# Performance work log

Measured on AMD Instinct MI355X. Metric: run time of the kernel, lower is better.

The kernel has to match this reference:

```python
import jax, jax.numpy as jnp
import numpy as np

TOP_K = 4


def setup_inputs() -> dict:
    key = jax.random.key(0)
    k1, k2, k3 = jax.random.split(key, 3)
    T, H, E = 16384, 2880, 128
    hidden_states = jax.random.normal(k1, (T, H), dtype=jnp.float32)
    weight = jax.random.normal(k2, (E, H), dtype=jnp.float32) * 0.02
    bias = jax.random.normal(k3, (E,), dtype=jnp.float32) * 0.02
    return {"hidden_states": hidden_states, "weight": weight, "bias": bias}


def reference(hidden_states, weight, bias):
    # [T, H] @ [H, E] + [E] -> router logits [T, E]
    hidden_states = hidden_states.reshape(-1, weight.shape[1])
    router_logits = jnp.einsum('th,eh->te', hidden_states, weight) + bias
    # top-k over experts, then softmax over the k selected logits
    router_top_value, router_indices = jax.lax.top_k(router_logits, TOP_K)
    router_scores = jax.nn.softmax(router_top_value, axis=-1)
    return router_scores, router_indices
```

## Files before the change

### kernel.cpp

```cpp
#include <hip/hip_runtime.h>
#include <hip/hip_bf16.h>
#include <math.h>

#define T_TOKENS 16384
#define H_DIM    2880
#define KHALF    1440
#define E_EXP    128
#define TOPK     4
#define MT       32
#define KC       32
#define EPS_GAP  5e-4f

typedef __bf16 bf16x8 __attribute__((ext_vector_type(8)));
typedef float  f32x4  __attribute__((ext_vector_type(4)));

__device__ __forceinline__ void split2(float a, float b,
                                       unsigned int& hi, unsigned int& lo) {
    float2 p; p.x = a; p.y = b;
    __hip_bfloat162 h = __float22bfloat162_rn(p);
    unsigned int hu; __builtin_memcpy(&hu, &h, 4);
    float2 r;
    r.x = a - __uint_as_float((hu & 0xffffu) << 16);
    r.y = b - __uint_as_float(hu & 0xffff0000u);
    __hip_bfloat162 l = __float22bfloat162_rn(r);
    unsigned int lu; __builtin_memcpy(&lu, &l, 4);
    hi = hu; lo = lu;
}

__global__ __launch_bounds__(512, 4) void router_main(
    const float* __restrict__ A, const float* __restrict__ W,
    const float* __restrict__ bias, float* __restrict__ out,
    int* __restrict__ flag_count, int* __restrict__ flag_list)
{
    __shared__ __align__(16) uint2 sAhi[2][2][128];
    __shared__ __align__(16) uint2 sAlo[2][2][128];
    __shared__ __align__(16) uint4 sWhi[2][8][64];
    __shared__ __align__(16) uint4 sWlo[2][8][64];
    __shared__ float sL[MT][129];

    const int tid    = threadIdx.x;
    const int t_base = blockIdx.x * MT;

    const int wave  = tid >> 6;
    const int L     = tid & 63;
    const int whalf = wave >> 2;
    const int wm    = wave & 1;
    const int wn    = (wave >> 1) & 1;

    const int shalf = tid >> 8;
    const int tid_h = tid & 255;
    const int at = tid_h >> 3;
    const int ac = tid_h & 7;
    const int a_idx = (at >> 4) * 128 + ((((ac >> 1) << 4) | (at & 15)) << 1) + (ac & 1);
    const float* Ag = A + (size_t)(t_base + at) * H_DIM + shalf * KHALF + ac * 4;
    const int we  = tid_h >> 1;
    const int wq0 = (tid_h & 1) * 2;
    const float* Wg = W + (size_t)we * H_DIM + shalf * KHALF + wq0 * 8;
    const int w_nt = we >> 4;
    const int w_n  = we & 15;

    uint2* sAhiF = &sAhi[shalf][0][0];
    uint2* sAloF = &sAlo[shalf][0][0];

    f32x4 acc[4];
#pragma unroll
    for (int i = 0; i < 4; ++i) { f32x4 z = {0.f, 0.f, 0.f, 0.f}; acc[i] = z; }

    for (int k0 = 0; k0 < KHALF; k0 += KC) {
        const float4 av  = *(const float4*)(Ag + k0);
        const float4 wv0 = *(const float4*)(Wg + k0);
        const float4 wv1 = *(const float4*)(Wg + k0 + 4);
        const float4 wv2 = *(const float4*)(Wg + k0 + 8);
        const float4 wv3 = *(const float4*)(Wg + k0 + 12);

        uint2 ahp, alp;
        split2(av.x, av.y, ahp.x, alp.x);
        split2(av.z, av.w, ahp.y, alp.y);

        uint4 whp0, wlp0, whp1, wlp1;
        split2(wv0.x, wv0.y, whp0.x, wlp0.x);
        split2(wv0.z, wv0.w, whp0.y, wlp0.y);
        split2(wv1.x, wv1.y, whp0.z, wlp0.z);
        split2(wv1.z, wv1.w, whp0.w, wlp0.w);
        split2(wv2.x, wv2.y, whp1.x, wlp1.x);
        split2(wv2.z, wv2.w, whp1.y, wlp1.y);
        split2(wv3.x, wv3.y, whp1.z, wlp1.z);
        split2(wv3.z, wv3.w, whp1.w, wlp1.w);

        __syncthreads();

        sAhiF[a_idx] = ahp;
        sAloF[a_idx] = alp;
        sWhi[shalf][w_nt][((wq0 + 0) << 4) | w_n] = whp0;
        sWhi[shalf][w_nt][((wq0 + 1) << 4) | w_n] = whp1;
        sWlo[shalf][w_nt][((wq0 + 0) << 4) | w_n] = wlp0;
        sWlo[shalf][w_nt][((wq0 + 1) << 4) | w_n] = wlp1;

        __syncthreads();

        const bf16x8 ahi = *(const bf16x8*)&sAhi[whalf][wm][L * 2];
        const bf16x8 alo = *(const bf16x8*)&sAlo[whalf][wm][L * 2];
#pragma unroll
        for (int i = 0; i < 4; ++i) {
            const int nt = wn * 4 + i;
            const bf16x8 whi = *(const bf16x8*)&sWhi[whalf][nt][L];
            const bf16x8 wlo = *(const bf16x8*)&sWlo[whalf][nt][L];
            acc[i] = __builtin_amdgcn_mfma_f32_16x16x32_bf16(ahi, whi, acc[i], 0, 0, 0);
            acc[i] = __builtin_amdgcn_mfma_f32_16x16x32_bf16(ahi, wlo, acc[i], 0, 0, 0);
            acc[i] = __builtin_amdgcn_mfma_f32_16x16x32_bf16(alo, whi, acc[i], 0, 0, 0);
        }
    }

    __syncthreads();
    if (whalf == 0) {
#pragma unroll
        for (int i = 0; i < 4; ++i) {
            const int e = wn * 64 + i * 16 + (L & 15);
            const float b = bias[e];
#pragma unroll
            for (int r = 0; r < 4; ++r)
                sL[wm * 16 + (L >> 4) * 4 + r][e] = acc[i][r] + b;
        }
    }
    __syncthreads();
    if (whalf == 1) {
#pragma unroll
        for (int i = 0; i < 4; ++i) {
            const int e = wn * 64 + i * 16 + (L & 15);
#pragma unroll
            for (int r = 0; r < 4; ++r)
                sL[wm * 16 + (L >> 4) * 4 + r][e] += acc[i][r];
        }
    }
    __syncthreads();

    if (tid < MT) {
        float v0 = -1e30f, v1 = -1e30f, v2 = -1e30f, v3 = -1e30f, v4 = -1e30f;
        int   i0 = 0, i1 = 0, i2 = 0, i3 = 0, i4 = 0;
        for (int e = 0; e < E_EXP; ++e) {
            const float x = sL[tid][e];
            if (x > v4) {
                if (x > v0)      { v4=v3;i4=i3; v3=v2;i3=i2; v2=v1;i2=i1; v1=v0;i1=i0; v0=x;i0=e; }
                else if (x > v1) { v4=v3;i4=i3; v3=v2;i3=i2; v2=v1;i2=i1; v1=x;i1=e; }
                else if (x > v2) { v4=v3;i4=i3; v3=v2;i3=i2; v2=x;i2=e; }
                else if (x > v3) { v4=v3;i4=i3; v3=x;i3=e; }
                else             { v4=x;i4=e; }
            }
        }
        const float g0 = v0 - v1, g1 = v1 - v2, g2 = v2 - v3, g3 = v3 - v4;
        float mg = g0 < g1 ? g0 : g1;
        mg = mg < g2 ? mg : g2;
        mg = mg < g3 ? mg : g3;

        const float e0x = expf(v0 - v0);
        const float e1x = expf(v1 - v0);
        const float e2x = expf(v2 - v0);
        const float e3x = expf(v3 - v0);
        const float s   = e0x + e1x + e2x + e3x;

        const int gt = t_base + tid;
        float* out_scores = out;
        float* out_idx    = out + (size_t)T_TOKENS * TOPK;
        out_scores[gt * 4 + 0] = e0x / s;
        out_scores[gt * 4 + 1] = e1x / s;
        out_scores[gt * 4 + 2] = e2x / s;
        out_scores[gt * 4 + 3] = e3x / s;
        out_idx[gt * 4 + 0] = (float)i0;
        out_idx[gt * 4 + 1] = (float)i1;
        out_idx[gt * 4 + 2] = (float)i2;
        out_idx[gt * 4 + 3] = (float)i3;

        if (mg < EPS_GAP) {
            const int p = atomicAdd(flag_count, 1);
            if (p < T_TOKENS) flag_list[p] = gt;
        }
    }
}

__global__ __launch_bounds__(256) void router_recheck(
    const float* __restrict__ A, const float* __restrict__ W,
    const float* __restrict__ bias, float* __restrict__ out,
    const int* __restrict__ flag_count, const int* __restrict__ flag_list)
{
    __shared__ double sPart[256];
    __shared__ double sLog[E_EXP];

    int count = *flag_count;
    if (count > T_TOKENS) count = T_TOKENS;

    const int tid = threadIdx.x;
    const int e   = tid & (E_EXP - 1);
    const int h   = tid >> 7;

    for (int i = blockIdx.x; i < count; i += gridDim.x) {
        const int t = flag_list[i];
        const float* arow = A + (size_t)t * H_DIM;
        const float* wrow = W + (size_t)e * H_DIM;
        const int k0 = h * (H_DIM / 2);

        double s0 = 0.0, s1 = 0.0, s2 = 0.0, s3 = 0.0;
        for (int k = k0; k < k0 + H_DIM / 2; k += 8) {
            const float4 a0 = *(const float4*)(arow + k);
            const float4 a1 = *(const float4*)(arow + k + 4);
            const float4 w0 = *(const float4*)(wrow + k);
            const float4 w1 = *(const float4*)(wrow + k + 4);
            s0 += (double)a0.x * (double)w0.x;
            s1 += (double)a0.y * (double)w0.y;
            s2 += (double)a0.z * (double)w0.z;
            s3 += (double)a0.w * (double)w0.w;
            s0 += (double)a1.x * (double)w1.x;
            s1 += (double)a1.y * (double)w1.y;
            s2 += (double)a1.z * (double)w1.z;
            s3 += (double)a1.w * (double)w1.w;
        }
        sPart[tid] = (s0 + s1) + (s2 + s3);
        __syncthreads();
        if (h == 0) sLog[e] = sPart[e] + sPart[e + 128] + (double)bias[e];
        __syncthreads();

        if (tid == 0) {
            double v0 = -1e300, v1 = -1e300, v2 = -1e300, v3 = -1e300;
            int    i0 = 0, i1 = 0, i2 = 0, i3 = 0;
            for (int q = 0; q < E_EXP; ++q) {
                const double x = sLog[q];
                if (x > v3) {
                    if (x > v0)      { v3=v2;i3=i2; v2=v1;i2=i1; v1=v0;i1=i0; v0=x;i0=q; }
                    else if (x > v1) { v3=v2;i3=i2; v2=v1;i2=i1; v1=x;i1=q; }
                    else if (x > v2) { v3=v2;i3=i2; v2=x;i2=q; }
                    else             { v3=x;i3=q; }
                }
            }
            const double e0x = exp(v0 - v0);
            const double e1x = exp(v1 - v0);
            const double e2x = exp(v2 - v0);
            const double e3x = exp(v3 - v0);
            const double s   = e0x + e1x + e2x + e3x;
            float* out_scores = out;
            float* out_idx    = out + (size_t)T_TOKENS * TOPK;
            out_scores[t * 4 + 0] = (float)(e0x / s);
            out_scores[t * 4 + 1] = (float)(e1x / s);
            out_scores[t * 4 + 2] = (float)(e2x / s);
            out_scores[t * 4 + 3] = (float)(e3x / s);
            out_idx[t * 4 + 0] = (float)i0;
            out_idx[t * 4 + 1] = (float)i1;
            out_idx[t * 4 + 2] = (float)i2;
            out_idx[t * 4 + 3] = (float)i3;
        }
        __syncthreads();
    }
}

extern "C" void kernel_launch(void* const* d_in, const int* in_sizes, int n_in,
                              void* d_out, int out_size, void* d_ws, size_t ws_size,
                              hipStream_t stream) {
    const float* A    = (const float*)d_in[0];
    const float* W    = (const float*)d_in[1];
    const float* bias = (const float*)d_in[2];
    float* out = (float*)d_out;

    int* flag_count = (int*)d_ws;
    int* flag_list  = (int*)d_ws + 1;

    hipMemsetAsync(flag_count, 0, sizeof(int), stream);
    router_main<<<dim3(T_TOKENS / MT), dim3(512), 0, stream>>>(A, W, bias, out,
                                                               flag_count, flag_list);
    router_recheck<<<dim3(256), dim3(256), 0, stream>>>(A, W, bias, out,
                                                        flag_count, flag_list);
}
```

Measured before the change: 392.0 us.

## Pre-split weights into bf16 hi/lo once and stream them via global_load_lds

Adds a prep kernel that splits W into bf16 hi/lo pairs once per call and stores them in the workspace in MFMA-ready tile order. The main kernel then copies the W tiles straight into LDS with global_load_lds, so each of the 512 blocks no longer redoes the W split or the register staging. It also prefetches the next A chunk after the barrier. The recheck kernel gets register double-buffered loads and a larger grid, and a fallback copy of the old kernel runs when the workspace is too small. The cost is an extra launch plus a larger workspace read of the pre-split weights.

```diff
diff --git a/kernel.cpp b/kernel.cpp
--- a/kernel.cpp
+++ b/kernel.cpp
@@ -9,7 +9,14 @@
 #define TOPK     4
 #define MT       32
 #define KC       32
+#define NCHUNK   (H_DIM / KC)
+#define NCHUNK_H (KHALF / KC)
 #define EPS_GAP  5e-4f
+
+#define WS_WOFF   64
+#define WS_WBYTES (NCHUNK * 1024 * 16)
+#define WS_FLOFF  (WS_WOFF + WS_WBYTES)
+#define WS_NEED   (WS_FLOFF + T_TOKENS * 4)
 
 typedef __bf16 bf16x8 __attribute__((ext_vector_type(8)));
 typedef float  f32x4  __attribute__((ext_vector_type(4)));
@@ -27,15 +34,35 @@
     hi = hu; lo = lu;
 }
 
+__global__ __launch_bounds__(256) void prep_w(const float* __restrict__ W,
+                                              uint4* __restrict__ wsW) {
+    const int f   = blockIdx.x * 256 + threadIdx.x;
+    const int kc  = f >> 9;
+    const int rem = f & 511;
+    const int nt  = rem >> 6;
+    const int L   = rem & 63;
+    const int e   = nt * 16 + (L & 15);
+    const int k   = kc * KC + (L >> 4) * 8;
+    const float* p = W + (size_t)e * H_DIM + k;
+    const float4 x0 = *(const float4*)p;
+    const float4 x1 = *(const float4*)(p + 4);
+    uint4 hi, lo;
+    split2(x0.x, x0.y, hi.x, lo.x);
+    split2(x0.z, x0.w, hi.y, lo.y);
+    split2(x1.x, x1.y, hi.z, lo.z);
+    split2(x1.z, x1.w, hi.w, lo.w);
+    wsW[(size_t)kc * 1024 + nt * 64 + L]       = hi;
+    wsW[(size_t)kc * 1024 + 512 + nt * 64 + L] = lo;
+}
+
 __global__ __launch_bounds__(512, 4) void router_main(
-    const float* __restrict__ A, const float* __restrict__ W,
+    const float* __restrict__ A, const uint4* __restrict__ wsW,
     const float* __restrict__ bias, float* __restrict__ out,
     int* __restrict__ flag_count, int* __restrict__ flag_list)
 {
     __shared__ __align__(16) uint2 sAhi[2][2][128];
     __shared__ __align__(16) uint2 sAlo[2][2][128];
-    __shared__ __align__(16) uint4 sWhi[2][8][64];
-    __shared__ __align__(16) uint4 sWlo[2][8][64];
+    __shared__ __align__(16) uint4 sW[2][1024];
     __shared__ float sL[MT][129];
 
     const int tid    = threadIdx.x;
@@ -53,11 +80,9 @@
     const int ac = tid_h & 7;
     const int a_idx = (at >> 4) * 128 + ((((ac >> 1) << 4) | (at & 15)) << 1) + (ac & 1);
     const float* Ag = A + (size_t)(t_base + at) * H_DIM + shalf * KHALF + ac * 4;
-    const int we  = tid_h >> 1;
-    const int wq0 = (tid_h & 1) * 2;
-    const float* Wg = W + (size_t)we * H_DIM + shalf * KHALF + wq0 * 8;
-    const int w_nt = we >> 4;
-    const int w_n  = we & 15;
+
+    const int wv = (wave & 3);
+    const uint4* wsrc = wsW + (size_t)(shalf * NCHUNK_H) * 1024 + (wv * 4) * 64 + L;
 
     uint2* sAhiF = &sAhi[shalf][0][0];
     uint2* sAloF = &sAlo[shalf][0][0];
@@ -66,45 +91,38 @@
 #pragma unroll
     for (int i = 0; i < 4; ++i) { f32x4 z = {0.f, 0.f, 0.f, 0.f}; acc[i] = z; }
 
-    for (int k0 = 0; k0 < KHALF; k0 += KC) {
-        const float4 av  = *(const float4*)(Ag + k0);
-        const float4 wv0 = *(const float4*)(Wg + k0);
-        const float4 wv1 = *(const float4*)(Wg + k0 + 4);
-        const float4 wv2 = *(const float4*)(Wg + k0 + 8);
-        const float4 wv3 = *(const float4*)(Wg + k0 + 12);
-
+    float4 av = *(const float4*)Ag;
+
+    for (int it = 0; it < NCHUNK_H; ++it) {
         uint2 ahp, alp;
         split2(av.x, av.y, ahp.x, alp.x);
         split2(av.z, av.w, ahp.y, alp.y);
 
-        uint4 whp0, wlp0, whp1, wlp1;
-        split2(wv0.x, wv0.y, whp0.x, wlp0.x);
-        split2(wv0.z, wv0.w, whp0.y, wlp0.y);
-        split2(wv1.x, wv1.y, whp0.z, wlp0.z);
-        split2(wv1.z, wv1.w, whp0.w, wlp0.w);
-        split2(wv2.x, wv2.y, whp1.x, wlp1.x);
-        split2(wv2.z, wv2.w, whp1.y, wlp1.y);
-        split2(wv3.x, wv3.y, whp1.z, wlp1.z);
-        split2(wv3.z, wv3.w, whp1.w, wlp1.w);
-
         __syncthreads();
 
         sAhiF[a_idx] = ahp;
         sAloF[a_idx] = alp;
-        sWhi[shalf][w_nt][((wq0 + 0) << 4) | w_n] = whp0;
-        sWhi[shalf][w_nt][((wq0 + 1) << 4) | w_n] = whp1;
-        sWlo[shalf][w_nt][((wq0 + 0) << 4) | w_n] = wlp0;
-        sWlo[shalf][w_nt][((wq0 + 1) << 4) | w_n] = wlp1;
-
-        __syncthreads();
+
+        const uint4* wc = wsrc + (size_t)it * 1024;
+#pragma unroll
+        for (int j = 0; j < 4; ++j) {
+            __builtin_amdgcn_global_load_lds(
+                (const __attribute__((address_space(1))) void*)(wc + j * 64),
+                (__attribute__((address_space(3))) void*)&sW[shalf][(wv * 4 + j) * 64],
+                16, 0, 0);
+        }
+
+        __syncthreads();
+
+        if (it + 1 < NCHUNK_H) av = *(const float4*)(Ag + (it + 1) * KC);
 
         const bf16x8 ahi = *(const bf16x8*)&sAhi[whalf][wm][L * 2];
         const bf16x8 alo = *(const bf16x8*)&sAlo[whalf][wm][L * 2];
 #pragma unroll
         for (int i = 0; i < 4; ++i) {
             const int nt = wn * 4 + i;
-            const bf16x8 whi = *(const bf16x8*)&sWhi[whalf][nt][L];
-            const bf16x8 wlo = *(const bf16x8*)&sWlo[whalf][nt][L];
+            const bf16x8 whi = *(const bf16x8*)&sW[whalf][nt * 64 + L];
+            const bf16x8 wlo = *(const bf16x8*)&sW[whalf][512 + nt * 64 + L];
             acc[i] = __builtin_amdgcn_mfma_f32_16x16x32_bf16(ahi, whi, acc[i], 0, 0, 0);
             acc[i] = __builtin_amdgcn_mfma_f32_16x16x32_bf16(ahi, wlo, acc[i], 0, 0, 0);
             acc[i] = __builtin_amdgcn_mfma_f32_16x16x32_bf16(alo, whi, acc[i], 0, 0, 0);
@@ -177,6 +195,151 @@
     }
 }
 
+__global__ __launch_bounds__(512, 4) void router_main_fb(
+    const float* __restrict__ A, const float* __restrict__ W,
+    const float* __restrict__ bias, float* __restrict__ out,
+    int* __restrict__ flag_count, int* __restrict__ flag_list)
+{
+    __shared__ __align__(16) uint2 sAhi[2][2][128];
+    __shared__ __align__(16) uint2 sAlo[2][2][128];
+    __shared__ __align__(16) uint4 sWhi[2][8][64];
+    __shared__ __align__(16) uint4 sWlo[2][8][64];
+    __shared__ float sL[MT][129];
+
+    const int tid    = threadIdx.x;
+    const int t_base = blockIdx.x * MT;
+    const int wave  = tid >> 6;
+    const int L     = tid & 63;
+    const int whalf = wave >> 2;
+    const int wm    = wave & 1;
+    const int wn    = (wave >> 1) & 1;
+    const int shalf = tid >> 8;
+    const int tid_h = tid & 255;
+    const int at = tid_h >> 3;
+    const int ac = tid_h & 7;
+    const int a_idx = (at >> 4) * 128 + ((((ac >> 1) << 4) | (at & 15)) << 1) + (ac & 1);
+    const float* Ag = A + (size_t)(t_base + at) * H_DIM + shalf * KHALF + ac * 4;
+    const int we  = tid_h >> 1;
+    const int wq0 = (tid_h & 1) * 2;
+    const float* Wg = W + (size_t)we * H_DIM + shalf * KHALF + wq0 * 8;
+    const int w_nt = we >> 4;
+    const int w_n  = we & 15;
+
+    uint2* sAhiF = &sAhi[shalf][0][0];
+    uint2* sAloF = &sAlo[shalf][0][0];
+
+    f32x4 acc[4];
+#pragma unroll
+    for (int i = 0; i < 4; ++i) { f32x4 z = {0.f, 0.f, 0.f, 0.f}; acc[i] = z; }
+
+    for (int k0 = 0; k0 < KHALF; k0 += KC) {
+        const float4 av  = *(const float4*)(Ag + k0);
+        const float4 wv0 = *(const float4*)(Wg + k0);
+        const float4 wv1 = *(const float4*)(Wg + k0 + 4);
+        const float4 wv2 = *(const float4*)(Wg + k0 + 8);
+        const float4 wv3 = *(const float4*)(Wg + k0 + 12);
+
+        uint2 ahp, alp;
+        split2(av.x, av.y, ahp.x, alp.x);
+        split2(av.z, av.w, ahp.y, alp.y);
+        uint4 whp0, wlp0, whp1, wlp1;
+        split2(wv0.x, wv0.y, whp0.x, wlp0.x);
+        split2(wv0.z, wv0.w, whp0.y, wlp0.y);
+        split2(wv1.x, wv1.y, whp0.z, wlp0.z);
+        split2(wv1.z, wv1.w, whp0.w, wlp0.w);
+        split2(wv2.x, wv2.y, whp1.x, wlp1.x);
+        split2(wv2.z, wv2.w, whp1.y, wlp1.y);
+        split2(wv3.x, wv3.y, whp1.z, wlp1.z);
+        split2(wv3.z, wv3.w, whp1.w, wlp1.w);
+
+        __syncthreads();
+        sAhiF[a_idx] = ahp;
+        sAloF[a_idx] = alp;
+        sWhi[shalf][w_nt][((wq0 + 0) << 4) | w_n] = whp0;
+        sWhi[shalf][w_nt][((wq0 + 1) << 4) | w_n] = whp1;
+        sWlo[shalf][w_nt][((wq0 + 0) << 4) | w_n] = wlp0;
+        sWlo[shalf][w_nt][((wq0 + 1) << 4) | w_n] = wlp1;
+        __syncthreads();
+
+        const bf16x8 ahi = *(const bf16x8*)&sAhi[whalf][wm][L * 2];
+        const bf16x8 alo = *(const bf16x8*)&sAlo[whalf][wm][L * 2];
+#pragma unroll
+        for (int i = 0; i < 4; ++i) {
+            const int nt = wn * 4 + i;
+            const bf16x8 whi = *(const bf16x8*)&sWhi[whalf][nt][L];
+            const bf16x8 wlo = *(const bf16x8*)&sWlo[whalf][nt][L];
+            acc[i] = __builtin_amdgcn_mfma_f32_16x16x32_bf16(ahi, whi, acc[i], 0, 0, 0);
+            acc[i] = __builtin_amdgcn_mfma_f32_16x16x32_bf16(ahi, wlo, acc[i], 0, 0, 0);
+            acc[i] = __builtin_amdgcn_mfma_f32_16x16x32_bf16(alo, whi, acc[i], 0, 0, 0);
+        }
+    }
+
+    __syncthreads();
+    if (whalf == 0) {
+#pragma unroll
+        for (int i = 0; i < 4; ++i) {
+            const int e = wn * 64 + i * 16 + (L & 15);
+            const float b = bias[e];
+#pragma unroll
+            for (int r = 0; r < 4; ++r)
+                sL[wm * 16 + (L >> 4) * 4 + r][e] = acc[i][r] + b;
+        }
+    }
+    __syncthreads();
+    if (whalf == 1) {
+#pragma unroll
+        for (int i = 0; i < 4; ++i) {
+            const int e = wn * 64 + i * 16 + (L & 15);
+#pragma unroll
+            for (int r = 0; r < 4; ++r)
+                sL[wm * 16 + (L >> 4) * 4 + r][e] += acc[i][r];
+        }
+    }
+    __syncthreads();
+
+    if (tid < MT) {
+        float v0 = -1e30f, v1 = -1e30f, v2 = -1e30f, v3 = -1e30f, v4 = -1e30f;
+        int   i0 = 0, i1 = 0, i2 = 0, i3 = 0, i4 = 0;
+        for (int e = 0; e < E_EXP; ++e) {
+            const float x = sL[tid][e];
+            if (x > v4) {
+                if (x > v0)      { v4=v3;i4=i3; v3=v2;i3=i2; v2=v1;i2=i1; v1=v0;i1=i0; v0=x;i0=e; }
+                else if (x > v1) { v4=v3;i4=i3; v3=v2;i3=i2; v2=v1;i2=i1; v1=x;i1=e; }
+                else if (x > v2) { v4=v3;i4=i3; v3=v2;i3=i2; v2=x;i2=e; }
+                else if (x > v3) { v4=v3;i4=i3; v3=x;i3=e; }
+                else             { v4=x;i4=e; }
+            }
+        }
+        const float g0 = v0 - v1, g1 = v1 - v2, g2 = v2 - v3, g3 = v3 - v4;
+        float mg = g0 < g1 ? g0 : g1;
+        mg = mg < g2 ? mg : g2;
+        mg = mg < g3 ? mg : g3;
+
+        const float e0x = expf(v0 - v0);
+        const float e1x = expf(v1 - v0);
+        const float e2x = expf(v2 - v0);
+        const float e3x = expf(v3 - v0);
+        const float s   = e0x + e1x + e2x + e3x;
+
+        const int gt = t_base + tid;
+        float* out_scores = out;
+        float* out_idx    = out + (size_t)T_TOKENS * TOPK;
+        out_scores[gt * 4 + 0] = e0x / s;
+        out_scores[gt * 4 + 1] = e1x / s;
+        out_scores[gt * 4 + 2] = e2x / s;
+        out_scores[gt * 4 + 3] = e3x / s;
+        out_idx[gt * 4 + 0] = (float)i0;
+        out_idx[gt * 4 + 1] = (float)i1;
+        out_idx[gt * 4 + 2] = (float)i2;
+        out_idx[gt * 4 + 3] = (float)i3;
+
+        if (mg < EPS_GAP) {
+            const int p = atomicAdd(flag_count, 1);
+            if (p < T_TOKENS) flag_list[p] = gt;
+        }
+    }
+}
+
 __global__ __launch_bounds__(256) void router_recheck(
     const float* __restrict__ A, const float* __restrict__ W,
     const float* __restrict__ bias, float* __restrict__ out,
@@ -194,24 +357,41 @@
 
     for (int i = blockIdx.x; i < count; i += gridDim.x) {
         const int t = flag_list[i];
-        const float* arow = A + (size_t)t * H_DIM;
-        const float* wrow = W + (size_t)e * H_DIM;
-        const int k0 = h * (H_DIM / 2);
+        const float* arow = A + (size_t)t * H_DIM + h * KHALF;
+        const float* wrow = W + (size_t)e * H_DIM + h * KHALF;
 
         double s0 = 0.0, s1 = 0.0, s2 = 0.0, s3 = 0.0;
-        for (int k = k0; k < k0 + H_DIM / 2; k += 8) {
-            const float4 a0 = *(const float4*)(arow + k);
-            const float4 a1 = *(const float4*)(arow + k + 4);
-            const float4 w0 = *(const float4*)(wrow + k);
-            const float4 w1 = *(const float4*)(wrow + k + 4);
-            s0 += (double)a0.x * (double)w0.x;
-            s1 += (double)a0.y * (double)w0.y;
-            s2 += (double)a0.z * (double)w0.z;
-            s3 += (double)a0.w * (double)w0.w;
-            s0 += (double)a1.x * (double)w1.x;
-            s1 += (double)a1.y * (double)w1.y;
-            s2 += (double)a1.z * (double)w1.z;
-            s3 += (double)a1.w * (double)w1.w;
+        float4 a[8], w[8];
+#pragma unroll
+        for (int q = 0; q < 8; ++q) {
+            a[q] = *(const float4*)(arow + q * 4);
+            w[q] = *(const float4*)(wrow + q * 4);
+        }
+        for (int it = 0; it < KHALF / 32 - 1; ++it) {
+            const float* ap = arow + (it + 1) * 32;
+            const float* wp = wrow + (it + 1) * 32;
+            float4 na[8], nw[8];
+#pragma unroll
+            for (int q = 0; q < 8; ++q) {
+                na[q] = *(const float4*)(ap + q * 4);
+                nw[q] = *(const float4*)(wp + q * 4);
+            }
+#pragma unroll
+            for (int q = 0; q < 8; ++q) {
+                s0 += (double)a[q].x * (double)w[q].x;
+                s1 += (double)a[q].y * (double)w[q].y;
+                s2 += (double)a[q].z * (double)w[q].z;
+                s3 += (double)a[q].w * (double)w[q].w;
+            }
+#pragma unroll
+            for (int q = 0; q < 8; ++q) { a[q] = na[q]; w[q] = nw[q]; }
+        }
+#pragma unroll
+        for (int q = 0; q < 8; ++q) {
+            s0 += (double)a[q].x * (double)w[q].x;
+            s1 += (double)a[q].y * (double)w[q].y;
+            s2 += (double)a[q].z * (double)w[q].z;
+            s3 += (double)a[q].w * (double)w[q].w;
         }
         sPart[tid] = (s0 + s1) + (s2 + s3);
         __syncthreads();
@@ -258,12 +438,23 @@
     const float* bias = (const float*)d_in[2];
     float* out = (float*)d_out;
 
-    int* flag_count = (int*)d_ws;
-    int* flag_list  = (int*)d_ws + 1;
-
-    hipMemsetAsync(flag_count, 0, sizeof(int), stream);
-    router_main<<<dim3(T_TOKENS / MT), dim3(512), 0, stream>>>(A, W, bias, out,
-                                                               flag_count, flag_list);
-    router_recheck<<<dim3(256), dim3(256), 0, stream>>>(A, W, bias, out,
-                                                        flag_count, flag_list);
-}
+    if (ws_size >= (size_t)WS_NEED) {
+        int*  flag_count = (int*)d_ws;
+        int*  flag_list  = (int*)((char*)d_ws + WS_FLOFF);
+        uint4* wsW       = (uint4*)((char*)d_ws + WS_WOFF);
+        hipMemsetAsync(flag_count, 0, sizeof(int), stream);
+        prep_w<<<dim3((NCHUNK * 512) / 256), dim3(256), 0, stream>>>(W, wsW);
+        router_main<<<dim3(T_TOKENS / MT), dim3(512), 0, stream>>>(A, wsW, bias, out,
+                                                                   flag_count, flag_list);
+        router_recheck<<<dim3(512), dim3(256), 0, stream>>>(A, W, bias, out,
+                                                            flag_count, flag_list);
+    } else {
+        int* flag_count = (int*)d_ws;
+        int* flag_list  = (int*)d_ws + 1;
+        hipMemsetAsync(flag_count, 0, sizeof(int), stream);
+        router_main_fb<<<dim3(T_TOKENS / MT), dim3(512), 0, stream>>>(A, W, bias, out,
+                                                                      flag_count, flag_list);
+        router_recheck<<<dim3(512), dim3(256), 0, stream>>>(A, W, bias, out,
+                                                            flag_count, flag_list);
+    }
+}
```

Measured after the change: 384.7 us. No clear change (-1.9%).
